# Optimization experiments

Measured on AMD Instinct MI355X. Metric: run time of the kernel, lower is better.

Reference implementation:

```python
import jax, jax.numpy as jnp
import numpy as np

NB_SITES = 16
K = 32            # nb_intervals
H = 512           # hidden_dim
EMB = 8           # embedding_dim
OUT = 3 * K + 3   # widths K + heights K + derivs K+1 + center_x + center_y
D = EMB * (NB_SITES - 1)
MIN_BIN = 1e-3
MIN_DER = 1e-3
B = 4096


def invsymlu(x):
    # inverse symmetric linear unit: x+1 for x>=0, 1/(1-x) for x<0
    return jnp.where(x >= 0, x + 1.0, 1.0 / (1.0 - x))


def freq_embed(x):
    # (...,) -> (..., EMB): 4 sin + 4 cos frequencies
    div = jnp.exp(jnp.arange(0, EMB, 2, dtype=jnp.float32) * (-jnp.log(100.0) / EMB))
    xe = x[..., None] * div
    return jnp.concatenate([jnp.sin(xe), jnp.cos(xe)], axis=-1)


def layernorm(x, s, b, eps=1e-6):
    m = jnp.mean(x, axis=-1, keepdims=True)
    v = jnp.var(x, axis=-1, keepdims=True)
    return (x - m) * jax.lax.rsqrt(v + eps) * s + b


def rqs_forward(inputs, uw, uh, ud, cx, cy):
    # inputs: (B,S); uw/uh: (B,S,K); ud: (B,S,K+1); cx/cy: (B,S)
    widths = MIN_BIN + invsymlu(uw)
    heights = MIN_BIN + invsymlu(uh)
    derivatives = MIN_DER + invsymlu(ud)

    pad = [(0, 0)] * (widths.ndim - 1) + [(1, 0)]
    cumwidths = jnp.pad(jnp.cumsum(widths, axis=-1), pad)
    cumwidths = cumwidths - cumwidths[..., -1:] / 2 + cx[..., None]
    cumheights = jnp.pad(jnp.cumsum(heights, axis=-1), pad)
    cumheights = cumheights - cumheights[..., -1:] / 2 + cy[..., None]

    left = inputs < cumwidths[..., 0]
    right = inputs >= cumwidths[..., -1]
    outputs = jnp.where(left, cumheights[..., 0] - (cumwidths[..., 0] - inputs) * derivatives[..., 0], 0.0)
    outputs = jnp.where(right, (inputs - cumwidths[..., -1]) * derivatives[..., -1] + cumheights[..., -1], outputs)
    logabsdet = jnp.where(left, jnp.log(derivatives[..., 0]), 0.0)
    logabsdet = jnp.where(right, jnp.log(derivatives[..., -1]), logabsdet)
    inside = ~(left | right)

    xs = jnp.where(inside, inputs, cx)
    # searchsorted via broadcast compare over K+1 knots
    bin_idx = (jnp.sum((xs[..., None] >= cumwidths), axis=-1) - 1)[..., None]

    take = lambda a: jnp.take_along_axis(a, bin_idx, axis=-1)[..., 0]
    icw = take(cumwidths)
    ibw = take(widths)
    ich = take(cumheights)
    delta = heights / widths
    idl = take(delta)
    ider = take(derivatives)
    iderp = take(derivatives[..., 1:])
    ih = take(heights)

    theta = (xs - icw) / ibw
    tomt = theta * (1 - theta)
    num = ih * (idl * theta ** 2 + ider * tomt)
    den = idl + (ider + iderp - 2 * idl) * tomt
    outputs = jnp.where(inside, ich + num / den, outputs)
    dnum = idl ** 2 * (iderp * theta ** 2 + 2 * idl * tomt + ider * (1 - theta) ** 2)
    logabsdet = jnp.where(inside, jnp.log(dnum) - 2 * jnp.log(den), logabsdet)
    return outputs, logabsdet


def setup_inputs() -> dict:
    ks = jax.random.split(jax.random.key(0), 8)
    S1 = NB_SITES - 1
    x = jax.random.normal(ks[0], (B, NB_SITES), jnp.float32)
    bias0 = jax.random.normal(ks[1], (OUT,), jnp.float32) * 0.1
    W0 = jax.random.normal(ks[2], (S1, D, H), jnp.float32) * (2.0 / D) ** 0.5
    W1 = jax.random.normal(ks[3], (S1, H, H), jnp.float32) * (2.0 / H) ** 0.5
    W2 = jax.random.normal(ks[4], (S1, H, H), jnp.float32) * (2.0 / H) ** 0.5
    Wf = jax.random.normal(ks[5], (S1, H, OUT), jnp.float32) * (2.0 / H) ** 0.5
    zH = jnp.zeros((S1, H), jnp.float32)
    oH = jnp.ones((S1, H), jnp.float32)
    return dict(x=x, bias0=bias0,
                W0=W0, b0=zH, ln0s=oH, ln0b=zH,
                W1=W1, b1=zH, ln1s=oH, ln1b=zH,
                W2=W2, b2=zH, ln2s=oH, ln2b=zH,
                Wf=Wf, bf=jnp.zeros((S1, OUT), jnp.float32))


def reference(x, bias0, W0, b0, ln0s, ln0b, W1, b1, ln1s, ln1b, W2, b2, ln2s, ln2b, Wf, bf):
    Bn = x.shape[0]
    S1 = NB_SITES - 1
    # embeddings of sites 0..S-2, flattened site-major: (B, D)
    e = freq_embed(x[:, :S1]).reshape(Bn, D)
    # causal per-site mask: site s (1..S-1) sees first EMB*s features
    site = jnp.arange(1, NB_SITES)
    mask = (jnp.arange(D)[None, :] < EMB * site[:, None]).astype(x.dtype)  # (S-1, D)
    Wm = W0 * mask[:, :, None]

    h = jnp.einsum('bd,sdh->bsh', e, Wm) + b0
    h = layernorm(jax.nn.gelu(h), ln0s, ln0b)
    y = jnp.einsum('bsh,shk->bsk', h, W1) + b1 + h   # residual
    y = layernorm(jax.nn.gelu(y), ln1s, ln1b)
    z = jnp.einsum('bsh,shk->bsk', y, W2) + b2 + y   # residual
    z = layernorm(jax.nn.gelu(z), ln2s, ln2b)
    p = jnp.einsum('bsh,sho->bso', z, Wf) + bf        # (B, S-1, OUT)

    p0 = jnp.broadcast_to(bias0, (Bn, 1, OUT))        # site 0: BiasOnlyNet
    params = jnp.concatenate([p0, p], axis=1)         # (B, S, OUT)

    uw = params[..., :K]
    uh = params[..., K:2 * K]
    ud = params[..., 2 * K:3 * K + 1]
    cx = params[..., 3 * K + 1]
    cy = params[..., 3 * K + 2]
    out, lad = rqs_forward(x, uw, uh, ud, cx, cy)
    return out, lad.sum(-1)
```

## Files before the change

### kernel.cpp

```cpp
#include <hip/hip_runtime.h>
#include <hip/hip_bf16.h>
#include <cstdint>
#include <cstddef>

typedef _Float16 f16;
typedef __attribute__((ext_vector_type(8))) _Float16 f16x8;
typedef __attribute__((ext_vector_type(4))) float f32x4;

#define DI __device__ __forceinline__

constexpr int BATCH  = 4096;
constexpr int S1     = 15;
constexpr int DPAD   = 128;
constexpr int H      = 512;
constexpr int OUTC   = 99;
constexpr int OUTPAD = 112;

DI float gelu_tanh(float x) {
  float t = 1.5957691216057308f * (x + 0.044715f * x * x * x);
  return x / (1.f + __expf(-t));
}

DI void gload16(const void* g, void* l) {
  __builtin_amdgcn_global_load_lds(
      (const __attribute__((address_space(1))) void*)g,
      (__attribute__((address_space(3))) void*)l, 16, 0, 0);
}

__global__ void embed_kernel(const float* __restrict__ x, f16* __restrict__ e) {
  const int b = blockIdx.x, d = threadIdx.x;
  float v = 0.f;
  if (d < 120) {
    const float divs[4] = {1.f, 0.31622776601683794f, 0.1f, 0.03162277660168379f};
    int site = d >> 3, j = d & 7;
    float arg = x[b * 16 + site] * divs[j & 3];
    v = (j < 4) ? sinf(arg) : cosf(arg);
  }
  e[b * DPAD + d] = (f16)v;
}

__global__ __launch_bounds__(256) void transpose_conv_kernel(
    const float* __restrict__ src, f16* __restrict__ dsth, f16* __restrict__ dstl,
    int K, int N, int Kpad, int Npad, int maskMul) {
  __shared__ float tile[32][33];
  const int s  = blockIdx.z;
  const int kb = blockIdx.x * 32, nb = blockIdx.y * 32;
  const int tx = threadIdx.x & 31, ty = threadIdx.x >> 5;
  for (int i = ty; i < 32; i += 8) {
    int k = kb + i, n = nb + tx;
    tile[i][tx] = (k < K && n < N) ? src[((size_t)s * K + k) * N + n] : 0.f;
  }
  __syncthreads();
  const int klim = maskMul ? maskMul * (s + 1) : 0x7FFFFFFF;
  for (int i = ty; i < 32; i += 8) {
    int n = nb + i, k = kb + tx;
    if (n < Npad && k < Kpad) {
      float v = (k < klim) ? tile[tx][i] : 0.f;
      size_t o = ((size_t)s * Npad + n) * Kpad + k;
      f16 h = (f16)v;
      dsth[o] = h;
      if (dstl) dstl[o] = (f16)(v - (float)h);
    }
  }
}

template<bool RES, bool SPLIT>
__global__ __launch_bounds__(512) void gemm_ln_kernel(
    const f16* __restrict__ A, const f16* __restrict__ Wh, const f16* __restrict__ Wl,
    const float* __restrict__ bias, const float* __restrict__ lns,
    const float* __restrict__ lnb, f16* __restrict__ out,
    int M, int Kd, int strideAS) {
  constexpr int BM = 64, BN = 512, BK = 64;
  constexpr int CPR = BK / 8, SWZ = CPR - 1;
  constexpr int WM = 32, WN = 128, FM = 2, FN = 8;
  extern __shared__ f16 smem[];
  f16* const As0 = smem;
  f16* const Bs0 = smem + 2 * BM * BK;

  const int n    = gridDim.x;
  const int b    = blockIdx.x;
  const int w    = (b & 7) * (n >> 3) + (b >> 3);
  const int srel = w >> 6;
  const int m0   = (w & 63) * BM;

  const f16* ap  = A  + (size_t)srel * strideAS + (size_t)m0 * Kd;
  const f16* wph = Wh + (size_t)srel * BN * Kd;
  const f16* wpl = SPLIT ? (Wl + (size_t)srel * BN * Kd) : nullptr;
  const int tid = threadIdx.x, wbase = tid & ~63;
  const int wave = tid >> 6, lane = tid & 63;
  const int wr = wave >> 2, wc = wave & 3;
  f32x4 acc[FM][FN] = {};
  const int laneRow = lane & 15;
  const int hi      = lane >> 4;

  {
    const int r = tid / CPR, c = tid % CPR, cg = c ^ (r & SWZ);
    gload16(ap + (size_t)r * Kd + cg * 8, As0 + (size_t)wbase * 8);
  }
#pragma unroll
  for (int base = 0; base < BN * CPR; base += 512) {
    const int idx = base + tid;
    const int r = idx / CPR, c = idx % CPR, cg = c ^ (r & SWZ);
    gload16(wph + (size_t)r * Kd + cg * 8, Bs0 + (size_t)(base + wbase) * 8);
  }
  __syncthreads();

  const int NT = Kd / BK;
  const int NV = SPLIT ? NT * 2 : NT;
  for (int v = 0; v < NV; ++v) {
    const int ktile = SPLIT ? (v >> 1) : v;
    f16* const Acur = As0 + (size_t)(ktile & 1) * BM * BK;
    f16* const Bcur = Bs0 + (size_t)(v & 1) * BN * BK;
    if (v + 1 < NV) {
      const int nk = SPLIT ? ((v + 1) >> 1) : (v + 1);
      const bool newTile = SPLIT ? (((v + 1) & 1) == 0) : true;
      if (newTile) {
        f16* const Anxt = As0 + (size_t)(nk & 1) * BM * BK;
        const int r = tid / CPR, c = tid % CPR, cg = c ^ (r & SWZ);
        gload16(ap + (size_t)r * Kd + nk * BK + cg * 8, Anxt + (size_t)wbase * 8);
      }
      const f16* src = (SPLIT && ((v + 1) & 1)) ? wpl : wph;
      f16* const Bnxt = Bs0 + (size_t)((v + 1) & 1) * BN * BK;
#pragma unroll
      for (int base = 0; base < BN * CPR; base += 512) {
        const int idx = base + tid;
        const int r = idx / CPR, c = idx % CPR, cg = c ^ (r & SWZ);
        gload16(src + (size_t)r * Kd + nk * BK + cg * 8, Bnxt + (size_t)(base + wbase) * 8);
      }
    }
#pragma unroll
    for (int kk = 0; kk < BK / 32; ++kk) {
      const int cc = kk * 4 + hi;
      f16x8 a[FM];
#pragma unroll
      for (int mi = 0; mi < FM; ++mi) {
        const int row = wr * WM + mi * 16 + laneRow;
        a[mi] = *reinterpret_cast<const f16x8*>(&Acur[row * BK + ((cc ^ (row & SWZ)) << 3)]);
      }
#pragma unroll
      for (int ni = 0; ni < FN; ++ni) {
        const int row = wc * WN + ni * 16 + laneRow;
        f16x8 bv = *reinterpret_cast<const f16x8*>(&Bcur[row * BK + ((cc ^ (row & SWZ)) << 3)]);
#pragma unroll
        for (int mi = 0; mi < FM; ++mi)
          acc[mi][ni] = __builtin_amdgcn_mfma_f32_16x16x32_f16(a[mi], bv, acc[mi][ni], 0, 0, 0);
      }
    }
    __syncthreads();
  }

  const int rbase = hi * 4;
  float bv[FN], sv[FN], bb[FN];
#pragma unroll
  for (int ni = 0; ni < FN; ++ni) {
    const int gn = wc * WN + ni * 16 + laneRow;
    bv[ni] = bias[srel * H + gn];
    sv[ni] = lns[srel * H + gn];
    bb[ni] = lnb[srel * H + gn];
  }
  float lsum[FM][4], lsq[FM][4];
#pragma unroll
  for (int mi = 0; mi < FM; ++mi)
#pragma unroll
    for (int r = 0; r < 4; ++r) { lsum[mi][r] = 0.f; lsq[mi][r] = 0.f; }
#pragma unroll
  for (int mi = 0; mi < FM; ++mi)
#pragma unroll
    for (int r = 0; r < 4; ++r) {
      const int row = wr * WM + mi * 16 + rbase + r;
#pragma unroll
      for (int ni = 0; ni < FN; ++ni) {
        const int gn = wc * WN + ni * 16 + laneRow;
        float y = acc[mi][ni][r] + bv[ni];
        if constexpr (RES)
          y += (float)A[(size_t)srel * strideAS + (size_t)(m0 + row) * Kd + gn];
        float g = gelu_tanh(y);
        acc[mi][ni][r] = g;
        lsum[mi][r] += g;
        lsq[mi][r]  += g * g;
      }
    }
#pragma unroll
  for (int o = 1; o < 16; o <<= 1)
#pragma unroll
    for (int mi = 0; mi < FM; ++mi)
#pragma unroll
      for (int r = 0; r < 4; ++r) {
        lsum[mi][r] += __shfl_xor(lsum[mi][r], o, 64);
        lsq[mi][r]  += __shfl_xor(lsq[mi][r], o, 64);
      }
  __syncthreads();
  float* red = reinterpret_cast<float*>(smem);
  if (laneRow == 0) {
#pragma unroll
    for (int mi = 0; mi < FM; ++mi)
#pragma unroll
      for (int r = 0; r < 4; ++r) {
        const int row = wr * WM + mi * 16 + rbase + r;
        red[(row * 4 + wc) * 2 + 0] = lsum[mi][r];
        red[(row * 4 + wc) * 2 + 1] = lsq[mi][r];
      }
  }
  __syncthreads();
#pragma unroll
  for (int mi = 0; mi < FM; ++mi)
#pragma unroll
    for (int r = 0; r < 4; ++r) {
      const int row = wr * WM + mi * 16 + rbase + r;
      float sum = 0.f, sq = 0.f;
#pragma unroll
      for (int w4 = 0; w4 < 4; ++w4) {
        sum += red[(row * 4 + w4) * 2 + 0];
        sq  += red[(row * 4 + w4) * 2 + 1];
      }
      const float mean = sum * (1.f / 512.f);
      const float var  = sq * (1.f / 512.f) - mean * mean;
      const float rstd = 1.f / sqrtf(var + 1e-6f);
#pragma unroll
      for (int ni = 0; ni < FN; ++ni) {
        const int gn = wc * WN + ni * 16 + laneRow;
        float z = (acc[mi][ni][r] - mean) * rstd * sv[ni] + bb[ni];
        out[((size_t)srel * M + m0 + row) * H + gn] = (f16)z;
      }
    }
}

__global__ __launch_bounds__(512) void gemm_out_kernel(
    const f16* __restrict__ A, const f16* __restrict__ Wh, const f16* __restrict__ Wl,
    const float* __restrict__ bias, float* __restrict__ out,
    int M, int Kd, int strideAS) {
  constexpr int BM = 128, BN = 112, BK = 64;
  constexpr int CPR = BK / 8, SWZ = CPR - 1;
  constexpr int FN = 7;
  extern __shared__ f16 smem[];
  f16* As  = smem;
  f16* Bhs = As + BM * BK;
  f16* Bls = Bhs + BN * BK;

  const int s  = blockIdx.z;
  const int m0 = blockIdx.x * BM;
  const f16* ap  = A  + (size_t)s * strideAS + (size_t)m0 * Kd;
  const f16* wph = Wh + (size_t)s * BN * Kd;
  const f16* wpl = Wl + (size_t)s * BN * Kd;
  const int tid = threadIdx.x, wbase = tid & ~63;
  const int wave = tid >> 6, lane = tid & 63;
  const int wr = wave;
  f32x4 acc[FN] = {};
  const int laneRow = lane & 15;
  const int hi      = lane >> 4;

  for (int k0 = 0; k0 < Kd; k0 += BK) {
    __syncthreads();
#pragma unroll
    for (int base = 0; base < BM * CPR; base += 512) {
      const int idx = base + tid;
      const int r = idx / CPR, c = idx % CPR, cg = c ^ (r & SWZ);
      gload16(ap + (size_t)r * Kd + k0 + cg * 8, As + (size_t)(base + wbase) * 8);
    }
#pragma unroll
    for (int base = 0; base < BN * CPR; base += 512) {
      const int idx = base + tid;
      if (idx < BN * CPR) {
        const int r = idx / CPR, c = idx % CPR, cg = c ^ (r & SWZ);
        const size_t go = (size_t)r * Kd + k0 + cg * 8;
        gload16(wph + go, Bhs + (size_t)(base + wbase) * 8);
        gload16(wpl + go, Bls + (size_t)(base + wbase) * 8);
      }
    }
    __syncthreads();
#pragma unroll
    for (int kk = 0; kk < BK / 32; ++kk) {
      const int cc = kk * 4 + hi;
      const int rowA = wr * 16 + laneRow;
      f16x8 a = *reinterpret_cast<const f16x8*>(&As[rowA * BK + ((cc ^ (rowA & SWZ)) << 3)]);
#pragma unroll
      for (int ni = 0; ni < FN; ++ni) {
        const int row = ni * 16 + laneRow;
        const int off = row * BK + ((cc ^ (row & SWZ)) << 3);
        f16x8 bh = *reinterpret_cast<const f16x8*>(&Bhs[off]);
        f16x8 bl = *reinterpret_cast<const f16x8*>(&Bls[off]);
        acc[ni] = __builtin_amdgcn_mfma_f32_16x16x32_f16(a, bh, acc[ni], 0, 0, 0);
        acc[ni] = __builtin_amdgcn_mfma_f32_16x16x32_f16(a, bl, acc[ni], 0, 0, 0);
      }
    }
  }

  const int rbase = hi * 4;
#pragma unroll
  for (int ni = 0; ni < FN; ++ni)
#pragma unroll
    for (int r = 0; r < 4; ++r) {
      const int gm = m0 + wr * 16 + rbase + r;
      const int gn = ni * 16 + laneRow;
      if (gn < OUTC)
        out[((size_t)s * M + gm) * OUTC + gn] = acc[ni][r] + bias[s * OUTC + gn];
    }
}

DI float invsymlu(float u) { return u >= 0.f ? u + 1.f : 1.f / (1.f - u); }

__global__ __launch_bounds__(128) void spline_kernel(
    const float* __restrict__ x, const float* __restrict__ bias0,
    const float* __restrict__ p, float* __restrict__ out0, float* __restrict__ ladbuf) {
  __shared__ float prm[128 * 101];
  const int i  = blockIdx.x;
  const int b0 = blockIdx.y * 128;
  if (i == 0) {
    for (int idx = threadIdx.x; idx < 128 * OUTC; idx += 128)
      prm[(idx / OUTC) * 101 + idx % OUTC] = bias0[idx % OUTC];
  } else {
    const float* src = p + ((size_t)(i - 1) * BATCH + b0) * OUTC;
    for (int idx = threadIdx.x; idx < 128 * OUTC; idx += 128)
      prm[(idx / OUTC) * 101 + idx % OUTC] = src[idx];
  }
  __syncthreads();
  const float* P = &prm[threadIdx.x * 101];
  const int b = b0 + threadIdx.x;
  const float inp = x[b * 16 + i];

  float tw = 0.f, th = 0.f;
  for (int k = 0; k < 32; ++k) tw += 0.001f + invsymlu(P[k]);
  for (int k = 0; k < 32; ++k) th += 0.001f + invsymlu(P[32 + k]);
  const float cx = P[97], cy = P[98];
  const float w0 = cx - 0.5f * tw, wK = cx + 0.5f * tw;
  const float h0 = cy - 0.5f * th, hK = cy + 0.5f * th;
  const float d0 = 0.001f + invsymlu(P[64]);
  const float dK = 0.001f + invsymlu(P[96]);
  float outv, lad;
  if (inp < w0) {
    outv = h0 - (w0 - inp) * d0;
    lad  = logf(d0);
  } else if (inp >= wK) {
    outv = (inp - wK) * dK + hK;
    lad  = logf(dK);
  } else {
    float run = w0, icw = w0, ibw = 1.f;
    int bin = 0;
    for (int k = 0; k < 32; ++k) {
      float wk = 0.001f + invsymlu(P[k]);
      if (inp >= run) { bin = k; icw = run; ibw = wk; }
      run += wk;
    }
    float runh = h0;
    for (int k = 0; k < bin; ++k) runh += 0.001f + invsymlu(P[32 + k]);
    const float ih    = 0.001f + invsymlu(P[32 + bin]);
    const float ich   = runh;
    const float ider  = 0.001f + invsymlu(P[64 + bin]);
    const float iderp = 0.001f + invsymlu(P[64 + bin + 1]);
    const float idl   = ih / ibw;
    const float theta = (inp - icw) / ibw;
    const float omt   = 1.f - theta;
    const float tomt  = theta * omt;
    const float num   = ih * (idl * theta * theta + ider * tomt);
    const float den   = idl + (ider + iderp - 2.f * idl) * tomt;
    outv = ich + num / den;
    const float dnum = idl * idl * (iderp * theta * theta + 2.f * idl * tomt + ider * omt * omt);
    lad = logf(dnum) - 2.f * logf(den);
  }
  out0[b * 16 + i]   = outv;
  ladbuf[b * 16 + i] = lad;
}

__global__ void lad_reduce_kernel(const float* __restrict__ ladbuf, float* __restrict__ out1) {
  const int b = blockIdx.x * 256 + threadIdx.x;
  float s = 0.f;
#pragma unroll
  for (int i = 0; i < 16; ++i) s += ladbuf[b * 16 + i];
  out1[b] = s;
}

extern "C" void kernel_launch(void* const* d_in, const int* in_sizes, int n_in,
                              void* d_out, int out_size, void* d_ws, size_t ws_size,
                              hipStream_t stream) {
  const float* x     = (const float*)d_in[0];
  const float* bias0 = (const float*)d_in[1];
  const float* W0    = (const float*)d_in[2];
  const float* b0    = (const float*)d_in[3];
  const float* ln0s  = (const float*)d_in[4];
  const float* ln0b  = (const float*)d_in[5];
  const float* W1    = (const float*)d_in[6];
  const float* b1    = (const float*)d_in[7];
  const float* ln1s  = (const float*)d_in[8];
  const float* ln1b  = (const float*)d_in[9];
  const float* W2    = (const float*)d_in[10];
  const float* b2    = (const float*)d_in[11];
  const float* ln2s  = (const float*)d_in[12];
  const float* ln2b  = (const float*)d_in[13];
  const float* Wf    = (const float*)d_in[14];
  const float* bfb   = (const float*)d_in[15];
  float* out0 = (float*)d_out;
  float* out1 = out0 + BATCH * 16;

  const size_t fixedBytes =
      (size_t)BATCH * DPAD * 2 +
      2 * ((size_t)S1 * H * DPAD * 2) +
      2 * ((size_t)S1 * H * H * 2) +
      2 * ((size_t)S1 * OUTPAD * H * 2) +
      (size_t)S1 * BATCH * OUTC * 4 +
      (size_t)BATCH * 16 * 4 +
      64 * 256;
  const size_t perSiteP = 2 * ((size_t)BATCH * H * 2);
  int CH = 1;
  if (ws_size > fixedBytes) {
    size_t c = (ws_size - fixedBytes) / perSiteP;
    CH = (c >= (size_t)S1) ? S1 : (c < 1 ? 1 : (int)c);
  }
  const int nPasses = (S1 + CH - 1) / CH;
  const int baseSz  = S1 / nPasses;
  const int remSz   = S1 % nPasses;

  char* ws = (char*)d_ws;
  size_t off = 0;
  auto take = [&](size_t bytes) {
    char* q = ws + off;
    off += (bytes + 255) & ~(size_t)255;
    return q;
  };
  f16* e     = (f16*)take((size_t)BATCH * DPAD * 2);
  f16* W0Th  = (f16*)take((size_t)S1 * H * DPAD * 2);
  f16* W0Tl  = (f16*)take((size_t)S1 * H * DPAD * 2);
  f16* W1Th  = (f16*)take((size_t)S1 * H * H * 2);
  f16* W2Th  = (f16*)take((size_t)S1 * H * H * 2);
  f16* WfTh  = (f16*)take((size_t)S1 * OUTPAD * H * 2);
  f16* WfTl  = (f16*)take((size_t)S1 * OUTPAD * H * 2);
  f16* P1    = (f16*)take((size_t)CH * BATCH * H * 2);
  f16* P2    = (f16*)take((size_t)CH * BATCH * H * 2);
  float* pbuf = (float*)take((size_t)S1 * BATCH * OUTC * 4);
  float* ladb = (float*)take((size_t)BATCH * 16 * 4);

  embed_kernel<<<BATCH, 128, 0, stream>>>(x, e);
  transpose_conv_kernel<<<dim3(4, 16, S1), 256, 0, stream>>>(W0, W0Th, W0Tl, 120, H, DPAD, H, 8);
  transpose_conv_kernel<<<dim3(16, 16, S1), 256, 0, stream>>>(W1, W1Th, nullptr, H, H, H, H, 0);
  transpose_conv_kernel<<<dim3(16, 16, S1), 256, 0, stream>>>(W2, W2Th, nullptr, H, H, H, H, 0);
  transpose_conv_kernel<<<dim3(16, 4, S1), 256, 0, stream>>>(Wf, WfTh, WfTl, H, OUTC, H, OUTPAD, 0);

  const size_t ldsFused = (size_t)(2 * 64 + 2 * 512) * 64 * 2;
  const size_t ldsOut   = (size_t)(128 + 112 + 112) * 64 * 2;

  int sb = 0;
  for (int pass = 0; pass < nPasses; ++pass) {
    const int nz = baseSz + (pass < remSz ? 1 : 0);
    const int gridFused = (BATCH / 64) * nz;
    gemm_ln_kernel<false, true><<<gridFused, 512, ldsFused, stream>>>(
        e, W0Th + (size_t)sb * H * DPAD, W0Tl + (size_t)sb * H * DPAD,
        b0 + sb * H, ln0s + sb * H, ln0b + sb * H, P2, BATCH, DPAD, 0);
    gemm_ln_kernel<true, false><<<gridFused, 512, ldsFused, stream>>>(
        P2, W1Th + (size_t)sb * H * H, nullptr,
        b1 + sb * H, ln1s + sb * H, ln1b + sb * H, P1, BATCH, H, BATCH * H);
    gemm_ln_kernel<true, false><<<gridFused, 512, ldsFused, stream>>>(
        P1, W2Th + (size_t)sb * H * H, nullptr,
        b2 + sb * H, ln2s + sb * H, ln2b + sb * H, P2, BATCH, H, BATCH * H);
    gemm_out_kernel<<<dim3(BATCH / 128, 1, nz), 512, ldsOut, stream>>>(
        P2, WfTh + (size_t)sb * OUTPAD * H, WfTl + (size_t)sb * OUTPAD * H,
        bfb + sb * OUTC, pbuf + (size_t)sb * BATCH * OUTC, BATCH, H, BATCH * H);
    sb += nz;
  }

  spline_kernel<<<dim3(16, 32), 128, 0, stream>>>(x, bias0, pbuf, out0, ladb);
  lad_reduce_kernel<<<BATCH / 256, 256, 0, stream>>>(ladb, out1);
}
```

Baseline: 292.7 us.

## Pipeline non-split GEMM-LN with 4-stage half-N B ring and vmcnt waits

For the residual hidden-layer GEMMs, the K loop is restructured to process the 512-wide N tile in two 256-column halves using a 4-slot B ring buffer and a 2-slot A buffer. Loads are issued two stages ahead, and each stage waits only on the oldest loads (s_waitcnt vmcnt) before one barrier, instead of a full __syncthreads per tile. The K-tile count becomes a compile-time template parameter so the loop fully unrolls, and the epilogue column mapping is remapped to match the half-N layout. This aims to hide global-to-LDS latency and cut barrier stalls, at the cost of hand-tuned wait counts that must match the exact number of outstanding loads.

```diff
diff --git a/kernel.cpp b/kernel.cpp
--- a/kernel.cpp
+++ b/kernel.cpp
@@ -25,6 +25,15 @@
   __builtin_amdgcn_global_load_lds(
       (const __attribute__((address_space(1))) void*)g,
       (__attribute__((address_space(3))) void*)l, 16, 0, 0);
+}
+
+template<int N>
+DI void waitv_barrier() {
+  if constexpr (N == 0)      asm volatile("s_waitcnt vmcnt(0)" ::: "memory");
+  else if constexpr (N == 4) asm volatile("s_waitcnt vmcnt(4)" ::: "memory");
+  else                       asm volatile("s_waitcnt vmcnt(5)" ::: "memory");
+  __builtin_amdgcn_s_barrier();
+  __builtin_amdgcn_sched_barrier(0);
 }
 
 __global__ void embed_kernel(const float* __restrict__ x, f16* __restrict__ e) {
@@ -64,7 +73,7 @@
   }
 }
 
-template<bool RES, bool SPLIT>
+template<int NTT, bool RES, bool SPLIT>
 __global__ __launch_bounds__(512) void gemm_ln_kernel(
     const f16* __restrict__ A, const f16* __restrict__ Wh, const f16* __restrict__ Wl,
     const float* __restrict__ bias, const float* __restrict__ lns,
@@ -74,8 +83,6 @@
   constexpr int CPR = BK / 8, SWZ = CPR - 1;
   constexpr int WM = 32, WN = 128, FM = 2, FN = 8;
   extern __shared__ f16 smem[];
-  f16* const As0 = smem;
-  f16* const Bs0 = smem + 2 * BM * BK;
 
   const int n    = gridDim.x;
   const int b    = blockIdx.x;
@@ -93,67 +100,137 @@
   const int laneRow = lane & 15;
   const int hi      = lane >> 4;
 
-  {
-    const int r = tid / CPR, c = tid % CPR, cg = c ^ (r & SWZ);
-    gload16(ap + (size_t)r * Kd + cg * 8, As0 + (size_t)wbase * 8);
-  }
-#pragma unroll
-  for (int base = 0; base < BN * CPR; base += 512) {
-    const int idx = base + tid;
-    const int r = idx / CPR, c = idx % CPR, cg = c ^ (r & SWZ);
-    gload16(wph + (size_t)r * Kd + cg * 8, Bs0 + (size_t)(base + wbase) * 8);
-  }
-  __syncthreads();
-
-  const int NT = Kd / BK;
-  const int NV = SPLIT ? NT * 2 : NT;
-  for (int v = 0; v < NV; ++v) {
-    const int ktile = SPLIT ? (v >> 1) : v;
-    f16* const Acur = As0 + (size_t)(ktile & 1) * BM * BK;
-    f16* const Bcur = Bs0 + (size_t)(v & 1) * BN * BK;
-    if (v + 1 < NV) {
-      const int nk = SPLIT ? ((v + 1) >> 1) : (v + 1);
-      const bool newTile = SPLIT ? (((v + 1) & 1) == 0) : true;
-      if (newTile) {
-        f16* const Anxt = As0 + (size_t)(nk & 1) * BM * BK;
-        const int r = tid / CPR, c = tid % CPR, cg = c ^ (r & SWZ);
-        gload16(ap + (size_t)r * Kd + nk * BK + cg * 8, Anxt + (size_t)wbase * 8);
-      }
-      const f16* src = (SPLIT && ((v + 1) & 1)) ? wpl : wph;
-      f16* const Bnxt = Bs0 + (size_t)((v + 1) & 1) * BN * BK;
-#pragma unroll
-      for (int base = 0; base < BN * CPR; base += 512) {
-        const int idx = base + tid;
-        const int r = idx / CPR, c = idx % CPR, cg = c ^ (r & SWZ);
-        gload16(src + (size_t)r * Kd + nk * BK + cg * 8, Bnxt + (size_t)(base + wbase) * 8);
-      }
-    }
-#pragma unroll
-    for (int kk = 0; kk < BK / 32; ++kk) {
-      const int cc = kk * 4 + hi;
-      f16x8 a[FM];
-#pragma unroll
-      for (int mi = 0; mi < FM; ++mi) {
-        const int row = wr * WM + mi * 16 + laneRow;
-        a[mi] = *reinterpret_cast<const f16x8*>(&Acur[row * BK + ((cc ^ (row & SWZ)) << 3)]);
-      }
-#pragma unroll
-      for (int ni = 0; ni < FN; ++ni) {
-        const int row = wc * WN + ni * 16 + laneRow;
-        f16x8 bv = *reinterpret_cast<const f16x8*>(&Bcur[row * BK + ((cc ^ (row & SWZ)) << 3)]);
-#pragma unroll
-        for (int mi = 0; mi < FM; ++mi)
-          acc[mi][ni] = __builtin_amdgcn_mfma_f32_16x16x32_f16(a[mi], bv, acc[mi][ni], 0, 0, 0);
-      }
+  if constexpr (SPLIT) {
+    f16* const As0 = smem;
+    f16* const Bs0 = smem + 2 * BM * BK;
+    {
+      const int r = tid / CPR, c = tid % CPR, cg = c ^ (r & SWZ);
+      gload16(ap + (size_t)r * Kd + cg * 8, As0 + (size_t)wbase * 8);
+    }
+#pragma unroll
+    for (int base = 0; base < BN * CPR; base += 512) {
+      const int idx = base + tid;
+      const int r = idx / CPR, c = idx % CPR, cg = c ^ (r & SWZ);
+      gload16(wph + (size_t)r * Kd + cg * 8, Bs0 + (size_t)(base + wbase) * 8);
     }
     __syncthreads();
+
+    const int NT = Kd / BK;
+    const int NV = NT * 2;
+    for (int v = 0; v < NV; ++v) {
+      const int ktile = v >> 1;
+      f16* const Acur = As0 + (size_t)(ktile & 1) * BM * BK;
+      f16* const Bcur = Bs0 + (size_t)(v & 1) * BN * BK;
+      if (v + 1 < NV) {
+        const int nk = (v + 1) >> 1;
+        const bool newTile = (((v + 1) & 1) == 0);
+        if (newTile) {
+          f16* const Anxt = As0 + (size_t)(nk & 1) * BM * BK;
+          const int r = tid / CPR, c = tid % CPR, cg = c ^ (r & SWZ);
+          gload16(ap + (size_t)r * Kd + nk * BK + cg * 8, Anxt + (size_t)wbase * 8);
+        }
+        const f16* src = ((v + 1) & 1) ? wpl : wph;
+        f16* const Bnxt = Bs0 + (size_t)((v + 1) & 1) * BN * BK;
+#pragma unroll
+        for (int base = 0; base < BN * CPR; base += 512) {
+          const int idx = base + tid;
+          const int r = idx / CPR, c = idx % CPR, cg = c ^ (r & SWZ);
+          gload16(src + (size_t)r * Kd + nk * BK + cg * 8, Bnxt + (size_t)(base + wbase) * 8);
+        }
+      }
+#pragma unroll
+      for (int kk = 0; kk < BK / 32; ++kk) {
+        const int cc = kk * 4 + hi;
+        f16x8 a[FM];
+#pragma unroll
+        for (int mi = 0; mi < FM; ++mi) {
+          const int row = wr * WM + mi * 16 + laneRow;
+          a[mi] = *reinterpret_cast<const f16x8*>(&Acur[row * BK + ((cc ^ (row & SWZ)) << 3)]);
+        }
+#pragma unroll
+        for (int ni = 0; ni < FN; ++ni) {
+          const int row = wc * WN + ni * 16 + laneRow;
+          f16x8 bv = *reinterpret_cast<const f16x8*>(&Bcur[row * BK + ((cc ^ (row & SWZ)) << 3)]);
+#pragma unroll
+          for (int mi = 0; mi < FM; ++mi)
+            acc[mi][ni] = __builtin_amdgcn_mfma_f32_16x16x32_f16(a[mi], bv, acc[mi][ni], 0, 0, 0);
+        }
+      }
+      __syncthreads();
+    }
+  } else {
+    f16* const ARb[2] = {smem, smem + BM * BK};
+    f16* const BRr[4] = {smem + 2 * BM * BK,
+                         smem + 2 * BM * BK + 1 * 256 * BK,
+                         smem + 2 * BM * BK + 2 * 256 * BK,
+                         smem + 2 * BM * BK + 3 * 256 * BK};
+
+    const int rA  = tid >> 3;
+    const int cg8 = (((tid & 7) ^ (rA & 7)) << 3);
+    const uint32_t offA = (uint32_t)rA * (uint32_t)Kd + cg8;
+    uint32_t offB[4];
+#pragma unroll
+    for (int j = 0; j < 4; ++j)
+      offB[j] = (uint32_t)(j * 64 + rA) * (uint32_t)Kd + cg8;
+    const uint32_t halfOff = (uint32_t)256 * (uint32_t)Kd;
+
+    gload16(ap + offA, ARb[0] + ((size_t)wbase << 3));
+#pragma unroll
+    for (int j = 0; j < 4; ++j)
+      gload16(wph + offB[j], BRr[0] + ((size_t)(j * 512 + wbase) << 3));
+#pragma unroll
+    for (int j = 0; j < 4; ++j)
+      gload16(wph + offB[j] + halfOff, BRr[1] + ((size_t)(j * 512 + wbase) << 3));
+
+    constexpr int NV = 2 * NTT;
+#pragma unroll
+    for (int p = 0; p < NV; ++p) {
+      if constexpr (true) {
+        if (p == NV - 1)      waitv_barrier<0>();
+        else if (p & 1)       waitv_barrier<5>();
+        else                  waitv_barrier<4>();
+      }
+      if (p + 2 < NV) {
+        const int t2 = (p + 2) >> 1, h2 = (p + 2) & 1;
+        if (h2 == 0)
+          gload16(ap + offA + (uint32_t)t2 * BK, ARb[t2 & 1] + ((size_t)wbase << 3));
+        f16* const Bn = BRr[(p + 2) & 3];
+        const uint32_t ko = (uint32_t)t2 * BK + (h2 ? halfOff : 0u);
+#pragma unroll
+        for (int j = 0; j < 4; ++j)
+          gload16(wph + offB[j] + ko, Bn + ((size_t)(j * 512 + wbase) << 3));
+      }
+      const f16* const Ab = ARb[(p >> 1) & 1];
+      const f16* const Bb = BRr[p & 3];
+      const int h = p & 1;
+#pragma unroll
+      for (int kk = 0; kk < BK / 32; ++kk) {
+        const int cc = kk * 4 + hi;
+        f16x8 a[FM];
+#pragma unroll
+        for (int mi = 0; mi < FM; ++mi) {
+          const int row = wr * WM + mi * 16 + laneRow;
+          a[mi] = *reinterpret_cast<const f16x8*>(&Ab[row * BK + ((cc ^ (row & 7)) << 3)]);
+        }
+#pragma unroll
+        for (int nl = 0; nl < 4; ++nl) {
+          const int rb = wc * 64 + nl * 16 + laneRow;
+          f16x8 bv = *reinterpret_cast<const f16x8*>(&Bb[rb * BK + ((cc ^ (rb & 7)) << 3)]);
+#pragma unroll
+          for (int mi = 0; mi < FM; ++mi)
+            acc[mi][h * 4 + nl] = __builtin_amdgcn_mfma_f32_16x16x32_f16(a[mi], bv, acc[mi][h * 4 + nl], 0, 0, 0);
+        }
+      }
+    }
+    __builtin_amdgcn_sched_barrier(0);
   }
 
   const int rbase = hi * 4;
   float bv[FN], sv[FN], bb[FN];
 #pragma unroll
   for (int ni = 0; ni < FN; ++ni) {
-    const int gn = wc * WN + ni * 16 + laneRow;
+    const int gn = SPLIT ? (wc * WN + ni * 16 + laneRow)
+                         : ((ni >> 2) * 256 + wc * 64 + (ni & 3) * 16 + laneRow);
     bv[ni] = bias[srel * H + gn];
     sv[ni] = lns[srel * H + gn];
     bb[ni] = lnb[srel * H + gn];
@@ -170,7 +247,8 @@
       const int row = wr * WM + mi * 16 + rbase + r;
 #pragma unroll
       for (int ni = 0; ni < FN; ++ni) {
-        const int gn = wc * WN + ni * 16 + laneRow;
+        const int gn = SPLIT ? (wc * WN + ni * 16 + laneRow)
+                             : ((ni >> 2) * 256 + wc * 64 + (ni & 3) * 16 + laneRow);
         float y = acc[mi][ni][r] + bv[ni];
         if constexpr (RES)
           y += (float)A[(size_t)srel * strideAS + (size_t)(m0 + row) * Kd + gn];
@@ -218,7 +296,8 @@
       const float rstd = 1.f / sqrtf(var + 1e-6f);
 #pragma unroll
       for (int ni = 0; ni < FN; ++ni) {
-        const int gn = wc * WN + ni * 16 + laneRow;
+        const int gn = SPLIT ? (wc * WN + ni * 16 + laneRow)
+                             : ((ni >> 2) * 256 + wc * 64 + (ni & 3) * 16 + laneRow);
         float z = (acc[mi][ni][r] - mean) * rstd * sv[ni] + bb[ni];
         out[((size_t)srel * M + m0 + row) * H + gn] = (f16)z;
       }
@@ -441,13 +520,13 @@
   for (int pass = 0; pass < nPasses; ++pass) {
     const int nz = baseSz + (pass < remSz ? 1 : 0);
     const int gridFused = (BATCH / 64) * nz;
-    gemm_ln_kernel<false, true><<<gridFused, 512, ldsFused, stream>>>(
+    gemm_ln_kernel<2, false, true><<<gridFused, 512, ldsFused, stream>>>(
         e, W0Th + (size_t)sb * H * DPAD, W0Tl + (size_t)sb * H * DPAD,
         b0 + sb * H, ln0s + sb * H, ln0b + sb * H, P2, BATCH, DPAD, 0);
-    gemm_ln_kernel<true, false><<<gridFused, 512, ldsFused, stream>>>(
+    gemm_ln_kernel<8, true, false><<<gridFused, 512, ldsFused, stream>>>(
         P2, W1Th + (size_t)sb * H * H, nullptr,
         b1 + sb * H, ln1s + sb * H, ln1b + sb * H, P1, BATCH, H, BATCH * H);
-    gemm_ln_kernel<true, false><<<gridFused, 512, ldsFused, stream>>>(
+    gemm_ln_kernel<8, true, false><<<gridFused, 512, ldsFused, stream>>>(
         P1, W2Th + (size_t)sb * H * H, nullptr,
         b2 + sb * H, ln2s + sb * H, ln2b + sb * H, P2, BATCH, H, BATCH * H);
     gemm_out_kernel<<<dim3(BATCH / 128, 1, nz), 512, ldsOut, stream>>>(
```

Result: slower. 299.3 us (+2.3%).
